# Performance work log

Measured on AMD Instinct MI355X. Metric: run time of the kernel, lower is better.

The kernel has to match this reference:

```python
import jax, jax.numpy as jnp
import numpy as np

N, NF1, NF2, NH, OUT, K = 16384, 2000, 10000, 512, 16, 19
BN_EPS = 1e-5

def _bn(x, g, b, m, v):
    # eval-mode BatchNorm1d with running stats
    return (x - m) * jax.lax.rsqrt(v + BN_EPS) * g + b


def setup_inputs() -> dict:
    key = jax.random.key(0)
    ks = jax.random.split(key, 24)
    f32 = jnp.float32
    def w(k, shape):
        return jax.random.normal(k, shape, f32) * 0.02
    inp = {
        "rna": jax.random.normal(ks[0], (N, NF1), f32),
        "atac": jax.random.normal(ks[1], (N, NF2), f32),
        "index_rna": jnp.arange(N, dtype=jnp.int32),
        "index_atac": jnp.arange(N, dtype=jnp.int32),
        "eps": jax.random.normal(ks[2], (N, OUT), f32),
        # RNA encoder
        "W_r1": w(ks[3], (NH, NF1)), "b_r1": jnp.zeros((NH,), f32),
        "g_r": jnp.ones((NH,), f32), "be_r": jnp.zeros((NH,), f32),
        "m_r": jnp.zeros((NH,), f32), "v_r": jnp.ones((NH,), f32),
        "W_rmu": w(ks[4], (OUT, NH)), "b_rmu": jnp.zeros((OUT,), f32),
        "W_rvar": w(ks[5], (OUT, NH)), "b_rvar": jnp.zeros((OUT,), f32),
        # ATAC encoder
        "W_a1": w(ks[6], (NH, NF2)), "b_a1": jnp.zeros((NH,), f32),
        "g_a": jnp.ones((NH,), f32), "be_a": jnp.zeros((NH,), f32),
        "m_a": jnp.zeros((NH,), f32), "v_a": jnp.ones((NH,), f32),
        "W_amu": w(ks[7], (OUT, NH)), "b_amu": jnp.zeros((OUT,), f32),
        "W_avar": w(ks[8], (OUT, NH)), "b_avar": jnp.zeros((OUT,), f32),
        # decoder
        "W_d1": w(ks[9], (NH, OUT)), "b_d1": jnp.zeros((NH,), f32),
        "g_d": jnp.ones((NH,), f32), "be_d": jnp.zeros((NH,), f32),
        "m_d": jnp.zeros((NH,), f32), "v_d": jnp.ones((NH,), f32),
        "W_d4": w(ks[10], (NF1 + NF2, NH)), "b_d4": jnp.zeros((NF1 + NF2,), f32),
        "cluster": jax.random.normal(ks[11], (K, OUT), f32),
    }
    return inp


def reference(rna, atac, index_rna, index_atac, eps,
              W_r1, b_r1, g_r, be_r, m_r, v_r, W_rmu, b_rmu, W_rvar, b_rvar,
              W_a1, b_a1, g_a, be_a, m_a, v_a, W_amu, b_amu, W_avar, b_avar,
              W_d1, b_d1, g_d, be_d, m_d, v_d, W_d4, b_d4, cluster):
    n = rna.shape[0]
    # encoders (dropout is identity in eval mode)
    h_rna = jax.nn.relu(_bn(rna @ W_r1.T + b_r1, g_r, be_r, m_r, v_r))
    zm_rna = h_rna @ W_rmu.T + b_rmu
    zv_rna = jnp.exp(h_rna @ W_rvar.T + b_rvar)
    h_atac = jax.nn.relu(_bn(atac @ W_a1.T + b_a1, g_a, be_a, m_a, v_a))
    zm_atac = h_atac @ W_amu.T + b_amu
    zv_atac = jnp.exp(h_atac @ W_avar.T + b_avar)
    # vectorized scatter replacing the per-sample Python loop
    mu = jnp.ones((n, 2, OUT), rna.dtype)
    var = jnp.ones((n, 2, OUT), rna.dtype)
    mask = jnp.zeros((n, 2, OUT), rna.dtype)
    mu = mu.at[index_rna, 0].set(zm_rna).at[index_atac, 1].set(zm_atac)
    var = var.at[index_rna, 0].set(zv_rna).at[index_atac, 1].set(zv_atac)
    mask = mask.at[index_rna, 0].set(1.0).at[index_atac, 1].set(1.0)
    # product of experts over the modality axis (axis=1)
    T = mask / var
    T_sum = T.sum(axis=1) + 1.0            # [n, OUT]
    z_mu = (mu * T).sum(axis=1) / T_sum
    z_var = 1.0 / T_sum
    # Normal(z_mu, scale=z_var).rsample() with externally supplied eps
    z = z_mu + z_var * eps
    # student-t style soft assignment to clusters
    d2 = jnp.sum((z[:, None, :] - cluster[None, :, :]) ** 2, axis=2)  # [n, K]
    q = 1.0 / (1.0 + d2)
    q = q / q.sum(axis=1, keepdims=True)
    # decoder
    h = jax.nn.relu(_bn(z @ W_d1.T + b_d1, g_d, be_d, m_d, v_d))
    recon_x = h @ W_d4.T + b_d4
    return (recon_x, z_mu, z_var, z, q)
```

## Files before the change

kernel.cpp:

```cpp
#include <hip/hip_runtime.h>
#include <hip/hip_bf16.h>

#define NS    16384
#define NF1c  2000
#define NF2c  10000
#define NH    512
#define KC    19
#define NREC  12000
#define NRECP 12032

typedef short bf16x8 __attribute__((ext_vector_type(8)));
typedef float f32x4  __attribute__((ext_vector_type(4)));

__device__ __forceinline__ unsigned short f2bf(float x) {
    return __builtin_bit_cast(unsigned short, __hip_bfloat16(x));
}
__device__ __forceinline__ float bf2f(unsigned short h) {
    return __builtin_bit_cast(float, (unsigned int)h << 16);
}

__device__ __forceinline__ void sync_nodrain() {
    asm volatile("s_waitcnt lgkmcnt(0)" ::: "memory");
    __builtin_amdgcn_s_barrier();
    asm volatile("" ::: "memory");
}

template<int BK> __device__ __forceinline__ int swz(int r) {
    return (BK == 32) ? ((r >> 1) & 3) : (r & 7);
}

__device__ __forceinline__ void gload16(const unsigned short* g, unsigned short* l) {
    __builtin_amdgcn_global_load_lds(
        (const __attribute__((address_space(1))) void*)g,
        (__attribute__((address_space(3))) void*)l, 16, 0, 0);
}

__global__ void k_cvt(const float* __restrict__ s, unsigned short* __restrict__ d, int n4) {
    int i = blockIdx.x * blockDim.x + threadIdx.x;
    int st = gridDim.x * blockDim.x;
    for (; i < n4; i += st) {
        float4 f = ((const float4*)s)[i];
        ushort4 o;
        o.x = f2bf(f.x); o.y = f2bf(f.y); o.z = f2bf(f.z); o.w = f2bf(f.w);
        ((ushort4*)d)[i] = o;
    }
}

__global__ void k_cvt_pad(const float* __restrict__ s, unsigned short* __restrict__ d,
                          int K, int Rv, long nchunks) {
    long i = (long)blockIdx.x * blockDim.x + threadIdx.x;
    const long stp = (long)gridDim.x * blockDim.x;
    const int Kp8 = K / 8;
    for (; i < nchunks; i += stp) {
        const long row = i / Kp8;
        const int  col = (int)(i - row * Kp8) * 8;
        __align__(16) unsigned short u[8] = {0, 0, 0, 0, 0, 0, 0, 0};
        if (row < Rv) {
            const float* p = s + row * (long)K + col;
            float4 f0 = *(const float4*)p;
            float4 f1 = *(const float4*)(p + 4);
            u[0] = f2bf(f0.x); u[1] = f2bf(f0.y); u[2] = f2bf(f0.z); u[3] = f2bf(f0.w);
            u[4] = f2bf(f1.x); u[5] = f2bf(f1.y); u[6] = f2bf(f1.z); u[7] = f2bf(f1.w);
        }
        *(uint4*)(d + row * (long)K + col) = *(uint4*)u;
    }
}

__global__ void k_prep_st(const float* __restrict__ g, const float* __restrict__ be,
                          const float* __restrict__ m, const float* __restrict__ v,
                          const float* __restrict__ b1,
                          float* __restrict__ s, float* __restrict__ t, int n) {
    int i = blockIdx.x * blockDim.x + threadIdx.x;
    if (i < n) {
        float sc = g[i] * rsqrtf(v[i] + 1e-5f);
        s[i] = sc;
        t[i] = be[i] + (b1[i] - m[i]) * sc;
    }
}

__global__ void k_zero(float* __restrict__ p, int n) {
    int i = blockIdx.x * blockDim.x + threadIdx.x;
    if (i < n) p[i] = 0.f;
}

__global__ __launch_bounds__(256)
void k_gemm(const void* __restrict__ Aptr, const unsigned short* __restrict__ B,
            int K, int Nn, int ntn,
            const float* __restrict__ sc, const float* __restrict__ sh,
            unsigned short* __restrict__ Hout)
{
    constexpr int BK = 64;
    constexpr int JC = BK / 16;
    __shared__ __align__(16) unsigned short As[2][128 * BK];
    __shared__ __align__(16) unsigned short Bs[2][128 * BK];

    const int nwg = gridDim.x;
    const int q8  = nwg >> 3;
    const int L   = (blockIdx.x & 7) * q8 + (blockIdx.x >> 3);
    const int tn  = L % ntn, tm = L / ntn;

    const int tid  = threadIdx.x;
    const int wave = tid >> 6, lane = tid & 63;
    const int wr   = wave >> 1, wc = wave & 1;
    const int lo   = lane & 15, hi = lane >> 4;
    const int srow = tid >> 1, shalf = tid & 1;
    const long arow = (long)tm * 128 + srow;
    const int  brow = tn * 128 + srow;
    const bool bok  = (brow < Nn);

    const float*          Af = (const float*)Aptr + arow * (long)K;
    const unsigned short* Bp = B + (long)brow * K;

    f32x4 acc[4][4];
#pragma unroll
    for (int i = 0; i < 4; i++)
#pragma unroll
        for (int j = 0; j < 4; j++) acc[i][j] = (f32x4){0.f, 0.f, 0.f, 0.f};

    float4 rfa[BK / 8];
    uint4  rb[JC];

    auto issue = [&](int k0, bool tail) {
        const int kb = k0 + shalf * (BK / 2);
        if (!tail) {
#pragma unroll
            for (int q = 0; q < BK / 8; q++) rfa[q] = *(const float4*)(Af + kb + q * 4);
        } else {
#pragma unroll
            for (int q = 0; q < BK / 8; q++) {
                float4 f;
                f.x = (kb + q * 4 + 0 < K) ? Af[kb + q * 4 + 0] : 0.f;
                f.y = (kb + q * 4 + 1 < K) ? Af[kb + q * 4 + 1] : 0.f;
                f.z = (kb + q * 4 + 2 < K) ? Af[kb + q * 4 + 2] : 0.f;
                f.w = (kb + q * 4 + 3 < K) ? Af[kb + q * 4 + 3] : 0.f;
                rfa[q] = f;
            }
        }
#pragma unroll
        for (int j = 0; j < JC; j++) rb[j] = (uint4){0, 0, 0, 0};
        if (bok) {
            if (!tail) {
#pragma unroll
                for (int j = 0; j < JC; j++) rb[j] = *(const uint4*)(Bp + kb + j * 8);
            } else {
#pragma unroll
                for (int j = 0; j < JC; j++) {
                    __align__(16) unsigned short t8[8];
#pragma unroll
                    for (int e = 0; e < 8; e++)
                        t8[e] = (kb + j * 8 + e < K) ? Bp[kb + j * 8 + e] : (unsigned short)0;
                    rb[j] = *(uint4*)t8;
                }
            }
        }
    };

    auto write = [&](int buf) {
        char* Ap = (char*)As[buf];
        char* Bq = (char*)Bs[buf];
        const int rbase = srow * (2 * BK);
        const int sw = swz<BK>(srow);
#pragma unroll
        for (int j = 0; j < JC; j++) {
            const int c = shalf * JC + j;
            const int pos = rbase + ((c ^ sw) << 4);
            uint4 av;
            unsigned int* w32 = (unsigned int*)&av;
            const float* fp = (const float*)&rfa[2 * j];
#pragma unroll
            for (int e = 0; e < 4; e++) {
                unsigned int l16 = f2bf(fp[2 * e]);
                unsigned int h16 = f2bf(fp[2 * e + 1]);
                w32[e] = l16 | (h16 << 16);
            }
            *(uint4*)(Ap + pos) = av;
            *(uint4*)(Bq + pos) = rb[j];
        }
    };

    auto comp = [&](int buf) {
        const char* Ap = (const char*)As[buf];
        const char* Bq = (const char*)Bs[buf];
#pragma unroll
        for (int s = 0; s < BK / 32; s++) {
            bf16x8 af[4], bfv[4];
#pragma unroll
            for (int f = 0; f < 4; f++) {
                const int ar = wr * 64 + f * 16 + lo;
                af[f]  = *(const bf16x8*)(Ap + ar * (2 * BK) + (((s * 4 + hi) ^ swz<BK>(ar)) << 4));
                const int br = wc * 64 + f * 16 + lo;
                bfv[f] = *(const bf16x8*)(Bq + br * (2 * BK) + (((s * 4 + hi) ^ swz<BK>(br)) << 4));
            }
#pragma unroll
            for (int i = 0; i < 4; i++)
#pragma unroll
                for (int j = 0; j < 4; j++)
                    acc[i][j] = __builtin_amdgcn_mfma_f32_16x16x32_bf16(af[i], bfv[j], acc[i][j], 0, 0, 0);
        }
    };

    const int ntf = K / BK;
    const bool rem = (K % BK) != 0;
    const int nt = ntf + (rem ? 1 : 0);
    issue(0, rem && nt == 1);
    for (int t = 0; t < nt; ++t) {
        write(t & 1);
        if (t + 1 < nt) issue((t + 1) * BK, rem && (t + 1 == nt - 1));
        sync_nodrain();
        comp(t & 1);
    }

#pragma unroll
    for (int i = 0; i < 4; i++) {
#pragma unroll
        for (int j = 0; j < 4; j++) {
            const int col = tn * 128 + wc * 64 + j * 16 + lo;
#pragma unroll
            for (int r = 0; r < 4; r++) {
                const long row = (long)tm * 128 + wr * 64 + i * 16 + hi * 4 + r;
                float v = fmaxf(acc[i][j][r] * sc[col] + sh[col], 0.f);
                Hout[row * NH + col] = f2bf(v);
            }
        }
    }
}

__global__ __launch_bounds__(512)
void k_rec256(const unsigned short* __restrict__ A, const unsigned short* __restrict__ B,
              const float* __restrict__ bias, float* __restrict__ Fout)
{
    __shared__ __align__(16) unsigned short As[2][256 * 32];
    __shared__ __align__(16) unsigned short Bs[2][256 * 32];

    const int q8 = gridDim.x >> 3;
    const int L  = (blockIdx.x & 7) * q8 + (blockIdx.x >> 3);
    const int tn = L % 47, tm = L / 47;

    const int tid  = threadIdx.x;
    const int w    = tid >> 6, lane = tid & 63;
    const int wm   = w >> 2, wn = w & 3;
    const int lo   = lane & 15, hi = lane >> 4;

    const int rl0 = w * 32 + (lane >> 2);
    const int sch = ((lane & 3) ^ ((lane >> 3) & 3)) * 8;
    const unsigned short* Adma = A + (size_t)(tm * 256 + rl0) * NH + sch;
    const unsigned short* Bdma = B + (size_t)(tn * 256 + rl0) * NH + sch;

    f32x4 acc[8][4];
#pragma unroll
    for (int i = 0; i < 8; i++)
#pragma unroll
        for (int j = 0; j < 4; j++) acc[i][j] = (f32x4){0.f, 0.f, 0.f, 0.f};

    auto issue = [&](int buf, int kt) {
        const int ko = kt * 32;
        gload16(Adma + ko,            &As[buf][(w * 32) * 32]);
        gload16(Adma + 16 * NH + ko,  &As[buf][(w * 32 + 16) * 32]);
        gload16(Bdma + ko,            &Bs[buf][(w * 32) * 32]);
        gload16(Bdma + 16 * NH + ko,  &Bs[buf][(w * 32 + 16) * 32]);
    };
    auto ldA = [&](int buf, int fm) -> bf16x8 {
        const int ar = wm * 128 + fm * 16 + lo;
        return *(const bf16x8*)((const char*)As[buf] + ar * 64 + ((hi ^ ((ar >> 1) & 3)) << 4));
    };
    auto ldB = [&](int buf, int fn) -> bf16x8 {
        const int br = wn * 64 + fn * 16 + lo;
        return *(const bf16x8*)((const char*)Bs[buf] + br * 64 + ((hi ^ ((br >> 1) & 3)) << 4));
    };

    const int nt = NH / 32;
    issue(0, 0);
    asm volatile("s_waitcnt vmcnt(0)" ::: "memory");
    __builtin_amdgcn_s_barrier();
    asm volatile("" ::: "memory");

    for (int kt = 0; kt < nt; ++kt) {
        const int cur = kt & 1;
        const bool more = (kt + 1 < nt);
        if (more) issue(cur ^ 1, kt + 1);
        bf16x8 bf[4], a0, a1, a2, a3;
#pragma unroll
        for (int fn = 0; fn < 4; fn++) bf[fn] = ldB(cur, fn);
        a0 = ldA(cur, 0); a1 = ldA(cur, 1); a2 = ldA(cur, 2); a3 = ldA(cur, 3);
        asm volatile("s_waitcnt lgkmcnt(0)" ::: "memory");
        __builtin_amdgcn_s_setprio(1);
#pragma unroll
        for (int fn = 0; fn < 4; fn++) {
            acc[0][fn] = __builtin_amdgcn_mfma_f32_16x16x32_bf16(a0, bf[fn], acc[0][fn], 0, 0, 0);
            acc[1][fn] = __builtin_amdgcn_mfma_f32_16x16x32_bf16(a1, bf[fn], acc[1][fn], 0, 0, 0);
            acc[2][fn] = __builtin_amdgcn_mfma_f32_16x16x32_bf16(a2, bf[fn], acc[2][fn], 0, 0, 0);
            acc[3][fn] = __builtin_amdgcn_mfma_f32_16x16x32_bf16(a3, bf[fn], acc[3][fn], 0, 0, 0);
        }
        __builtin_amdgcn_s_setprio(0);
        a0 = ldA(cur, 4); a1 = ldA(cur, 5); a2 = ldA(cur, 6); a3 = ldA(cur, 7);
        asm volatile("s_waitcnt lgkmcnt(0)" ::: "memory");
        __builtin_amdgcn_s_setprio(1);
#pragma unroll
        for (int fn = 0; fn < 4; fn++) {
            acc[4][fn] = __builtin_amdgcn_mfma_f32_16x16x32_bf16(a0, bf[fn], acc[4][fn], 0, 0, 0);
            acc[5][fn] = __builtin_amdgcn_mfma_f32_16x16x32_bf16(a1, bf[fn], acc[5][fn], 0, 0, 0);
            acc[6][fn] = __builtin_amdgcn_mfma_f32_16x16x32_bf16(a2, bf[fn], acc[6][fn], 0, 0, 0);
            acc[7][fn] = __builtin_amdgcn_mfma_f32_16x16x32_bf16(a3, bf[fn], acc[7][fn], 0, 0, 0);
        }
        __builtin_amdgcn_s_setprio(0);
        if (more) {
            asm volatile("s_waitcnt vmcnt(0)" ::: "memory");
            __builtin_amdgcn_s_barrier();
            asm volatile("" ::: "memory");
        }
    }

#pragma unroll
    for (int fm = 0; fm < 8; fm++) {
#pragma unroll
        for (int fn = 0; fn < 4; fn++) {
            const int col = tn * 256 + wn * 64 + fn * 16 + lo;
#pragma unroll
            for (int r = 0; r < 4; r++) {
                const long row = (long)tm * 256 + wm * 128 + fm * 16 + hi * 4 + r;
                if (col < NREC)
                    __builtin_nontemporal_store(acc[fm][fn][r] + bias[col],
                                                &Fout[row * (long)NREC + col]);
            }
        }
    }
}

__global__ __launch_bounds__(256)
void k_proj(const unsigned short* __restrict__ h_rna,
            const unsigned short* __restrict__ h_atac,
            const float* __restrict__ W_rmu, const float* __restrict__ b_rmu,
            const float* __restrict__ W_rvar, const float* __restrict__ b_rvar,
            const float* __restrict__ W_amu, const float* __restrict__ b_amu,
            const float* __restrict__ W_avar, const float* __restrict__ b_avar,
            const int* __restrict__ idx_rna, const int* __restrict__ idx_atac,
            float* __restrict__ mu0, float* __restrict__ var0,
            float* __restrict__ mu1, float* __restrict__ var1,
            float* __restrict__ mflag)
{
    __shared__ __align__(16) unsigned short hsh[4][2][NH];
    const int wave = threadIdx.x >> 6, lane = threadIdx.x & 63;
    const long i = (long)blockIdx.x * 4 + wave;
    *(uint4*)&hsh[wave][0][lane * 8] = *(const uint4*)(h_rna  + i * NH + lane * 8);
    *(uint4*)&hsh[wave][1][lane * 8] = *(const uint4*)(h_atac + i * NH + lane * 8);
    __syncthreads();
    const int mod = lane >> 5, oo = lane & 31;
    const int isv = oo >> 4, o = oo & 15;
    const float *W, *bias;
    if (mod == 0) { W = isv ? W_rvar : W_rmu; bias = isv ? b_rvar : b_rmu; }
    else          { W = isv ? W_avar : W_amu; bias = isv ? b_avar : b_amu; }
    const unsigned short* hr = hsh[wave][mod];
    const float* wrow = W + o * NH;
    float a = 0.f;
#pragma unroll 4
    for (int k = 0; k < NH; k += 4) {
        float4 w = *(const float4*)(wrow + k);
        a += bf2f(hr[k]) * w.x + bf2f(hr[k+1]) * w.y + bf2f(hr[k+2]) * w.z + bf2f(hr[k+3]) * w.w;
    }
    a += bias[o];
    const int tgt = (mod == 0) ? idx_rna[i] : idx_atac[i];
    float* mu  = mod ? mu1  : mu0;
    float* var = mod ? var1 : var0;
    if (!isv) mu[(long)tgt * 16 + o] = a;
    else      var[(long)tgt * 16 + o] = expf(a);
    if (oo == 0) mflag[(long)mod * NS + tgt] = 1.f;
}

__global__ __launch_bounds__(256)
void k_combine(const float* __restrict__ mu0, const float* __restrict__ var0,
               const float* __restrict__ mu1, const float* __restrict__ var1,
               const float* __restrict__ mflag,
               const float* __restrict__ eps, const float* __restrict__ cluster,
               const float* __restrict__ W_d1,
               const float* __restrict__ s_d, const float* __restrict__ t_d,
               float* __restrict__ o_zmu, float* __restrict__ o_zvar,
               float* __restrict__ o_z, float* __restrict__ o_q,
               unsigned short* __restrict__ h_d)
{
    __shared__ float zsh[4][16];
    const int wave = threadIdx.x >> 6, lane = threadIdx.x & 63;
    const long i = (long)blockIdx.x * 4 + wave;
    if (lane < 16) {
        const int d = lane;
        const float f0 = mflag[i], f1 = mflag[NS + i];
        float ts = 1.f, num = 0.f;
        if (f0 != 0.f) { float iv = 1.f / var0[i*16+d]; ts += iv; num += mu0[i*16+d] * iv; }
        if (f1 != 0.f) { float iv = 1.f / var1[i*16+d]; ts += iv; num += mu1[i*16+d] * iv; }
        const float zm = num / ts, zv = 1.f / ts;
        const float z = zm + zv * eps[i*16+d];
        o_zmu[i*16+d] = zm; o_zvar[i*16+d] = zv; o_z[i*16+d] = z;
        zsh[wave][d] = z;
    }
    __syncthreads();
    float zreg[16];
#pragma unroll
    for (int d = 0; d < 16; d++) zreg[d] = zsh[wave][d];
    float qk = 0.f;
    if (lane < KC) {
        float d2 = 0.f;
#pragma unroll
        for (int d = 0; d < 16; d++) { float df = zreg[d] - cluster[lane*16+d]; d2 += df*df; }
        qk = 1.f / (1.f + d2);
    }
    float ssum = qk;
#pragma unroll
    for (int off = 16; off > 0; off >>= 1) ssum += __shfl_xor(ssum, off, 32);
    if (lane < KC) o_q[i * KC + lane] = qk / ssum;
#pragma unroll
    for (int j = 0; j < 8; j++) {
        const int c = lane + 64 * j;
        float a = 0.f;
#pragma unroll
        for (int d = 0; d < 16; d += 4) {
            float4 w = *(const float4*)(W_d1 + c * 16 + d);
            a += zreg[d] * w.x + zreg[d+1] * w.y + zreg[d+2] * w.z + zreg[d+3] * w.w;
        }
        a = fmaxf(a * s_d[c] + t_d[c], 0.f);
        h_d[i * NH + c] = f2bf(a);
    }
}

extern "C" void kernel_launch(void* const* d_in, const int* in_sizes, int n_in,
                              void* d_out, int out_size, void* d_ws, size_t ws_size,
                              hipStream_t stream)
{
    const float* rna    = (const float*)d_in[0];
    const float* atac   = (const float*)d_in[1];
    const int*   i_rna  = (const int*)d_in[2];
    const int*   i_atac = (const int*)d_in[3];
    const float* eps    = (const float*)d_in[4];
    const float* W_r1   = (const float*)d_in[5];
    const float* b_r1   = (const float*)d_in[6];
    const float* g_r    = (const float*)d_in[7];
    const float* be_r   = (const float*)d_in[8];
    const float* m_r    = (const float*)d_in[9];
    const float* v_r    = (const float*)d_in[10];
    const float* W_rmu  = (const float*)d_in[11];
    const float* b_rmu  = (const float*)d_in[12];
    const float* W_rvar = (const float*)d_in[13];
    const float* b_rvar = (const float*)d_in[14];
    const float* W_a1   = (const float*)d_in[15];
    const float* b_a1   = (const float*)d_in[16];
    const float* g_a    = (const float*)d_in[17];
    const float* be_a   = (const float*)d_in[18];
    const float* m_a    = (const float*)d_in[19];
    const float* v_a    = (const float*)d_in[20];
    const float* W_amu  = (const float*)d_in[21];
    const float* b_amu  = (const float*)d_in[22];
    const float* W_avar = (const float*)d_in[23];
    const float* b_avar = (const float*)d_in[24];
    const float* W_d1   = (const float*)d_in[25];
    const float* b_d1   = (const float*)d_in[26];
    const float* g_d    = (const float*)d_in[27];
    const float* be_d   = (const float*)d_in[28];
    const float* m_d    = (const float*)d_in[29];
    const float* v_d    = (const float*)d_in[30];
    const float* W_d4   = (const float*)d_in[31];
    const float* b_d4   = (const float*)d_in[32];
    const float* clus   = (const float*)d_in[33];
    (void)in_sizes; (void)n_in; (void)out_size;

    char* w = (char*)d_ws;
    size_t off = 0;
    auto carve = [&](size_t bytes) { void* p = w + off; off += (bytes + 255) & ~(size_t)255; return p; };
    unsigned short* wr1b  = (unsigned short*)carve((size_t)NH * NF1c * 2);
    unsigned short* wa1b  = (unsigned short*)carve((size_t)NH * NF2c * 2);
    unsigned short* wd4b  = (unsigned short*)carve((size_t)NRECP * NH * 2);
    unsigned short* hrna  = (unsigned short*)carve((size_t)NS * NH * 2);
    unsigned short* hatac = (unsigned short*)carve((size_t)NS * NH * 2);
    unsigned short* hd    = (unsigned short*)carve((size_t)NS * NH * 2);
    float* mu0   = (float*)carve((size_t)NS * 16 * 4);
    float* var0  = (float*)carve((size_t)NS * 16 * 4);
    float* mu1   = (float*)carve((size_t)NS * 16 * 4);
    float* var1  = (float*)carve((size_t)NS * 16 * 4);
    float* mflag = (float*)carve((size_t)2 * NS * 4);
    float* st    = (float*)carve((size_t)6 * NH * 4);
    if (off > ws_size) return;

    float* s_r = st;          float* t_r = st + NH;
    float* s_a = st + 2*NH;   float* t_a = st + 3*NH;
    float* s_d = st + 4*NH;   float* t_d = st + 5*NH;

    float* out    = (float*)d_out;
    float* o_rec  = out;
    float* o_zmu  = out + (size_t)NS * NREC;
    float* o_zvar = o_zmu + (size_t)NS * 16;
    float* o_z    = o_zvar + (size_t)NS * 16;
    float* o_q    = o_z + (size_t)NS * 16;

    k_cvt<<<1024, 256, 0, stream>>>(W_r1, wr1b, NH * NF1c / 4);
    k_cvt<<<2048, 256, 0, stream>>>(W_a1, wa1b, NH * NF2c / 4);
    k_cvt_pad<<<2048, 256, 0, stream>>>(W_d4, wd4b, NH, NREC, (long)NRECP * (NH / 8));
    k_prep_st<<<2, 256, 0, stream>>>(g_r, be_r, m_r, v_r, b_r1, s_r, t_r, NH);
    k_prep_st<<<2, 256, 0, stream>>>(g_a, be_a, m_a, v_a, b_a1, s_a, t_a, NH);
    k_prep_st<<<2, 256, 0, stream>>>(g_d, be_d, m_d, v_d, b_d1, s_d, t_d, NH);
    k_zero<<<(2 * NS + 255) / 256, 256, 0, stream>>>(mflag, 2 * NS);

    dim3 blk(256);
    k_gemm<<<512, blk, 0, stream>>>(rna,  wr1b, NF1c, NH, 4, s_r, t_r, hrna);
    k_gemm<<<512, blk, 0, stream>>>(atac, wa1b, NF2c, NH, 4, s_a, t_a, hatac);
    k_proj<<<NS / 4, blk, 0, stream>>>(hrna, hatac, W_rmu, b_rmu, W_rvar, b_rvar,
                                       W_amu, b_amu, W_avar, b_avar, i_rna, i_atac,
                                       mu0, var0, mu1, var1, mflag);
    k_combine<<<NS / 4, blk, 0, stream>>>(mu0, var0, mu1, var1, mflag, eps, clus,
                                          W_d1, s_d, t_d, o_zmu, o_zvar, o_z, o_q, hd);
    k_rec256<<<3008, dim3(512), 0, stream>>>(hd, wd4b, b_d4, o_rec);
}
```

Measured before the change: 1.196 ms.

## Fuse prep kernels and run both encoder GEMMs in one interleaved launch

```diff
diff --git a/kernel.cpp b/kernel.cpp
--- a/kernel.cpp
+++ b/kernel.cpp
@@ -35,81 +35,103 @@
         (__attribute__((address_space(3))) void*)l, 16, 0, 0);
 }
 
-__global__ void k_cvt(const float* __restrict__ s, unsigned short* __restrict__ d, int n4) {
-    int i = blockIdx.x * blockDim.x + threadIdx.x;
-    int st = gridDim.x * blockDim.x;
-    for (; i < n4; i += st) {
-        float4 f = ((const float4*)s)[i];
-        ushort4 o;
-        o.x = f2bf(f.x); o.y = f2bf(f.y); o.z = f2bf(f.z); o.w = f2bf(f.w);
-        ((ushort4*)d)[i] = o;
-    }
-}
-
-__global__ void k_cvt_pad(const float* __restrict__ s, unsigned short* __restrict__ d,
-                          int K, int Rv, long nchunks) {
+#define C1 128000L
+#define C2 768000L
+#define C3 1538048L
+#define C4 1539584L
+#define C5 1547776L
+__global__ void k_prep(const float* __restrict__ W_r1, unsigned short* __restrict__ wr1b,
+                       const float* __restrict__ W_a1, unsigned short* __restrict__ wa1b,
+                       const float* __restrict__ W_d4, unsigned short* __restrict__ wd4b,
+                       const float* __restrict__ g_r, const float* __restrict__ be_r,
+                       const float* __restrict__ m_r, const float* __restrict__ v_r,
+                       const float* __restrict__ b_r1,
+                       const float* __restrict__ g_a, const float* __restrict__ be_a,
+                       const float* __restrict__ m_a, const float* __restrict__ v_a,
+                       const float* __restrict__ b_a1,
+                       const float* __restrict__ g_d, const float* __restrict__ be_d,
+                       const float* __restrict__ m_d, const float* __restrict__ v_d,
+                       const float* __restrict__ b_d1,
+                       float* __restrict__ st, float* __restrict__ mflag)
+{
     long i = (long)blockIdx.x * blockDim.x + threadIdx.x;
     const long stp = (long)gridDim.x * blockDim.x;
-    const int Kp8 = K / 8;
-    for (; i < nchunks; i += stp) {
-        const long row = i / Kp8;
-        const int  col = (int)(i - row * Kp8) * 8;
-        __align__(16) unsigned short u[8] = {0, 0, 0, 0, 0, 0, 0, 0};
-        if (row < Rv) {
-            const float* p = s + row * (long)K + col;
+    for (; i < C5; i += stp) {
+        if (i < C2) {
+            const float* src; unsigned short* dst; long j; int kp8;
+            if (i < C1) { src = W_r1; dst = wr1b; j = i;      kp8 = NF1c / 8; }
+            else        { src = W_a1; dst = wa1b; j = i - C1; kp8 = NF2c / 8; }
+            const long row = j / kp8;
+            const int  col = (int)(j - row * kp8) * 8;
+            const float* p = src + row * (long)(kp8 * 8) + col;
             float4 f0 = *(const float4*)p;
             float4 f1 = *(const float4*)(p + 4);
+            __align__(16) unsigned short u[8];
             u[0] = f2bf(f0.x); u[1] = f2bf(f0.y); u[2] = f2bf(f0.z); u[3] = f2bf(f0.w);
             u[4] = f2bf(f1.x); u[5] = f2bf(f1.y); u[6] = f2bf(f1.z); u[7] = f2bf(f1.w);
-        }
-        *(uint4*)(d + row * (long)K + col) = *(uint4*)u;
-    }
-}
-
-__global__ void k_prep_st(const float* __restrict__ g, const float* __restrict__ be,
-                          const float* __restrict__ m, const float* __restrict__ v,
-                          const float* __restrict__ b1,
-                          float* __restrict__ s, float* __restrict__ t, int n) {
-    int i = blockIdx.x * blockDim.x + threadIdx.x;
-    if (i < n) {
-        float sc = g[i] * rsqrtf(v[i] + 1e-5f);
-        s[i] = sc;
-        t[i] = be[i] + (b1[i] - m[i]) * sc;
-    }
-}
-
-__global__ void k_zero(float* __restrict__ p, int n) {
-    int i = blockIdx.x * blockDim.x + threadIdx.x;
-    if (i < n) p[i] = 0.f;
+            *(uint4*)(dst + row * (long)(kp8 * 8) + col) = *(uint4*)u;
+        } else if (i < C3) {
+            const long j = i - C2;
+            const long row = j >> 6;
+            const int  col = (int)(j & 63) * 8;
+            __align__(16) unsigned short u[8] = {0, 0, 0, 0, 0, 0, 0, 0};
+            if (row < NREC) {
+                const float* p = W_d4 + row * (long)NH + col;
+                float4 f0 = *(const float4*)p;
+                float4 f1 = *(const float4*)(p + 4);
+                u[0] = f2bf(f0.x); u[1] = f2bf(f0.y); u[2] = f2bf(f0.z); u[3] = f2bf(f0.w);
+                u[4] = f2bf(f1.x); u[5] = f2bf(f1.y); u[6] = f2bf(f1.z); u[7] = f2bf(f1.w);
+            }
+            *(uint4*)(wd4b + row * (long)NH + col) = *(uint4*)u;
+        } else if (i < C4) {
+            const int j = (int)(i - C3);
+            const int which = j >> 9, o = j & 511;
+            const float *g, *be, *m, *v, *b1;
+            if (which == 0)      { g = g_r; be = be_r; m = m_r; v = v_r; b1 = b_r1; }
+            else if (which == 1) { g = g_a; be = be_a; m = m_a; v = v_a; b1 = b_a1; }
+            else                 { g = g_d; be = be_d; m = m_d; v = v_d; b1 = b_d1; }
+            const float sc = g[o] * rsqrtf(v[o] + 1e-5f);
+            st[which * 2 * NH + o]      = sc;
+            st[which * 2 * NH + NH + o] = be[o] + (b1[o] - m[o]) * sc;
+        } else {
+            const long j = i - C4;
+            ((float4*)mflag)[j] = make_float4(0.f, 0.f, 0.f, 0.f);
+        }
+    }
 }
 
 __global__ __launch_bounds__(256)
-void k_gemm(const void* __restrict__ Aptr, const unsigned short* __restrict__ B,
-            int K, int Nn, int ntn,
-            const float* __restrict__ sc, const float* __restrict__ sh,
-            unsigned short* __restrict__ Hout)
+void k_encf(const float* __restrict__ A_a, const float* __restrict__ A_r,
+            const unsigned short* __restrict__ B_a, const unsigned short* __restrict__ B_r,
+            const float* __restrict__ st,
+            unsigned short* __restrict__ H_a, unsigned short* __restrict__ H_r)
 {
     constexpr int BK = 64;
     constexpr int JC = BK / 16;
     __shared__ __align__(16) unsigned short As[2][128 * BK];
     __shared__ __align__(16) unsigned short Bs[2][128 * BK];
 
-    const int nwg = gridDim.x;
-    const int q8  = nwg >> 3;
-    const int L   = (blockIdx.x & 7) * q8 + (blockIdx.x >> 3);
-    const int tn  = L % ntn, tm = L / ntn;
+    const int q8 = gridDim.x >> 3;
+    const int L  = (blockIdx.x & 7) * q8 + (blockIdx.x >> 3);
+    const int which = L & 1;
+    const int inner = L >> 1;
+    const int tn = inner & 3, tm = inner >> 2;
+
+    const float*          Ag = which ? A_r : A_a;
+    const unsigned short* Bg = which ? B_r : B_a;
+    const int K = which ? NF1c : NF2c;
+    const float* sc = st + (which ? 0 : 2 * NH);
+    const float* sh = sc + NH;
+    unsigned short* Hout = which ? H_r : H_a;
 
     const int tid  = threadIdx.x;
     const int wave = tid >> 6, lane = tid & 63;
     const int wr   = wave >> 1, wc = wave & 1;
     const int lo   = lane & 15, hi = lane >> 4;
     const int srow = tid >> 1, shalf = tid & 1;
-    const long arow = (long)tm * 128 + srow;
-    const int  brow = tn * 128 + srow;
-    const bool bok  = (brow < Nn);
-
-    const float*          Af = (const float*)Aptr + arow * (long)K;
-    const unsigned short* Bp = B + (long)brow * K;
+
+    const float*          Af = Ag + (size_t)(tm * 128 + srow) * K;
+    const unsigned short* Bp = Bg + (size_t)(tn * 128 + srow) * K;
 
     f32x4 acc[4][4];
 #pragma unroll
@@ -125,6 +147,8 @@
         if (!tail) {
 #pragma unroll
             for (int q = 0; q < BK / 8; q++) rfa[q] = *(const float4*)(Af + kb + q * 4);
+#pragma unroll
+            for (int j = 0; j < JC; j++) rb[j] = *(const uint4*)(Bp + kb + j * 8);
         } else {
 #pragma unroll
             for (int q = 0; q < BK / 8; q++) {
@@ -135,22 +159,13 @@
                 f.w = (kb + q * 4 + 3 < K) ? Af[kb + q * 4 + 3] : 0.f;
                 rfa[q] = f;
             }
-        }
-#pragma unroll
-        for (int j = 0; j < JC; j++) rb[j] = (uint4){0, 0, 0, 0};
-        if (bok) {
-            if (!tail) {
-#pragma unroll
-                for (int j = 0; j < JC; j++) rb[j] = *(const uint4*)(Bp + kb + j * 8);
-            } else {
-#pragma unroll
-                for (int j = 0; j < JC; j++) {
-                    __align__(16) unsigned short t8[8];
-#pragma unroll
-                    for (int e = 0; e < 8; e++)
-                        t8[e] = (kb + j * 8 + e < K) ? Bp[kb + j * 8 + e] : (unsigned short)0;
-                    rb[j] = *(uint4*)t8;
-                }
+#pragma unroll
+            for (int j = 0; j < JC; j++) {
+                __align__(16) unsigned short t8[8];
+#pragma unroll
+                for (int e = 0; e < 8; e++)
+                    t8[e] = (kb + j * 8 + e < K) ? Bp[kb + j * 8 + e] : (unsigned short)0;
+                rb[j] = *(uint4*)t8;
             }
         }
     };
@@ -477,9 +492,9 @@
     float* st    = (float*)carve((size_t)6 * NH * 4);
     if (off > ws_size) return;
 
-    float* s_r = st;          float* t_r = st + NH;
-    float* s_a = st + 2*NH;   float* t_a = st + 3*NH;
-    float* s_d = st + 4*NH;   float* t_d = st + 5*NH;
+    float* s_a = st + 2 * NH; float* t_a = st + 3 * NH;
+    float* s_d = st + 4 * NH; float* t_d = st + 5 * NH;
+    (void)s_a; (void)t_a;
 
     float* out    = (float*)d_out;
     float* o_rec  = out;
@@ -488,17 +503,13 @@
     float* o_z    = o_zvar + (size_t)NS * 16;
     float* o_q    = o_z + (size_t)NS * 16;
 
-    k_cvt<<<1024, 256, 0, stream>>>(W_r1, wr1b, NH * NF1c / 4);
-    k_cvt<<<2048, 256, 0, stream>>>(W_a1, wa1b, NH * NF2c / 4);
-    k_cvt_pad<<<2048, 256, 0, stream>>>(W_d4, wd4b, NH, NREC, (long)NRECP * (NH / 8));
-    k_prep_st<<<2, 256, 0, stream>>>(g_r, be_r, m_r, v_r, b_r1, s_r, t_r, NH);
-    k_prep_st<<<2, 256, 0, stream>>>(g_a, be_a, m_a, v_a, b_a1, s_a, t_a, NH);
-    k_prep_st<<<2, 256, 0, stream>>>(g_d, be_d, m_d, v_d, b_d1, s_d, t_d, NH);
-    k_zero<<<(2 * NS + 255) / 256, 256, 0, stream>>>(mflag, 2 * NS);
-
     dim3 blk(256);
-    k_gemm<<<512, blk, 0, stream>>>(rna,  wr1b, NF1c, NH, 4, s_r, t_r, hrna);
-    k_gemm<<<512, blk, 0, stream>>>(atac, wa1b, NF2c, NH, 4, s_a, t_a, hatac);
+    k_prep<<<4096, blk, 0, stream>>>(W_r1, wr1b, W_a1, wa1b, W_d4, wd4b,
+                                     g_r, be_r, m_r, v_r, b_r1,
+                                     g_a, be_a, m_a, v_a, b_a1,
+                                     g_d, be_d, m_d, v_d, b_d1,
+                                     st, mflag);
+    k_encf<<<1024, blk, 0, stream>>>(atac, rna, wa1b, wr1b, st, hatac, hrna);
     k_proj<<<NS / 4, blk, 0, stream>>>(hrna, hatac, W_rmu, b_rmu, W_rvar, b_rvar,
                                        W_amu, b_amu, W_avar, b_avar, i_rna, i_atac,
                                        mu0, var0, mu1, var1, mflag);
```

New measurement: 1.440 ms. 20.4% more time.
